# Kernel tuning notes

Hardware: AMD Instinct MI355X
Metric: run time of the kernel (lower is better)

Reference implementation:

```python
import jax, jax.numpy as jnp
import numpy as np

N, K, D = 131072, 1024, 128
COMMITMENT_COST = 0.25


def setup_inputs() -> dict:
    key = jax.random.key(0)
    k1, k2 = jax.random.split(key)
    c_input = jax.random.normal(k1, (N, D), dtype=jnp.float32)
    # nn.Embedding weight initialized N(0, 0.1)
    embedding_weight = jax.random.normal(k2, (K, D), dtype=jnp.float32) * 0.1
    return {"c_input": c_input, "embedding_weight": embedding_weight}


def reference(c_input, embedding_weight):
    distances = (
        jnp.sum(c_input ** 2, axis=1, keepdims=True)
        + jnp.sum(embedding_weight ** 2, axis=1)
        - 2.0 * jnp.matmul(c_input, embedding_weight.T)
    )
    encoding_indices = jnp.argmin(distances, axis=1)  # [N]
    encodings = jax.nn.one_hot(encoding_indices, K, dtype=c_input.dtype)  # [N, K]
    # one-hot @ weight == direct gather
    quantized = embedding_weight[encoding_indices]  # [N, D]
    e_latent_loss = jnp.mean((jax.lax.stop_gradient(quantized) - c_input) ** 2)
    q_latent_loss = jnp.mean((quantized - jax.lax.stop_gradient(c_input)) ** 2)
    loss = q_latent_loss + COMMITMENT_COST * e_latent_loss
    # straight-through estimator
    quantized_st = c_input + jax.lax.stop_gradient(quantized - c_input)
    return (loss, quantized_st, encodings)
```

## Files before the change

kernel.cpp:

```cpp
#include <hip/hip_runtime.h>
#include <hip/hip_bf16.h>

#define NROWS 131072
#define KC 1024
#define DD 128
#define MARGIN 1e-3f

typedef __attribute__((ext_vector_type(8))) short short8;
typedef __attribute__((ext_vector_type(4))) float f32x4;

__device__ inline short f2bf_hi(float f) {
  unsigned u = __builtin_bit_cast(unsigned, f);
  u += 0x7fffu + ((u >> 16) & 1u);
  return (short)(u >> 16);
}
__device__ inline float bf2f(short s) {
  unsigned u = ((unsigned)(unsigned short)s) << 16;
  return __builtin_bit_cast(float, u);
}

__global__ void vq_prep(const float* __restrict__ E, short* __restrict__ EH,
                        short* __restrict__ EL, float* __restrict__ SE,
                        float* __restrict__ out) {
  int b = blockIdx.x, t = threadIdx.x;
  if (b < 64) {
    int idx = b * 256 + t;
    int s = (idx >> 6) & 3, l = idx & 63;
    int c = idx >> 8;
    int q = l >> 4, n = l & 15;
    const float* src = E + (16 * c + n) * DD + 32 * s + 8 * q;
    short8 h, lo;
#pragma unroll
    for (int j = 0; j < 8; ++j) {
      float x = src[j];
      short hb = f2bf_hi(x);
      h[j] = hb;
      lo[j] = f2bf_hi(x - bf2f(hb));
    }
    *(short8*)(EH + idx * 8) = h;
    *(short8*)(EL + idx * 8) = lo;
  } else {
    if (t == 0) out[0] = 0.f;
    for (int k = t; k < KC; k += 256) {
      double acc = 0.0;
      const float* er = E + k * DD;
      for (int i = 0; i < DD; ++i) { double v = (double)er[i]; acc += v * v; }
      SE[k] = (float)acc;
    }
  }
}

__global__ __launch_bounds__(256, 2) void vq_main(
    const float* __restrict__ X, const float* __restrict__ E,
    const short* __restrict__ EH, const short* __restrict__ EL,
    const float* __restrict__ SE, float* __restrict__ out) {
  __shared__ __align__(16) short lbh[16384];
  __shared__ __align__(16) short lbl[16384];
  __shared__ int lidx[128];
  __shared__ int lflag[128];
  __shared__ int lany;
  __shared__ float lx[128];
  __shared__ float lrv[256];
  __shared__ int lri[256];
  __shared__ float lsx;
  __shared__ float lloss[4];

  const int tid = threadIdx.x;
  const int w = tid >> 6, l = tid & 63, q = l >> 4, n = l & 15;
  const int row_base = blockIdx.x * 128;
  if (tid == 0) lany = 0;

  short8 ah[2][4], al[2][4];
#pragma unroll
  for (int mt = 0; mt < 2; ++mt) {
    const float* xp = X + (row_base + 32 * w + 16 * mt + n) * DD + 8 * q;
#pragma unroll
    for (int s = 0; s < 4; ++s) {
      f32x4 x0 = *(const f32x4*)(xp + 32 * s);
      f32x4 x1 = *(const f32x4*)(xp + 32 * s + 4);
#pragma unroll
      for (int j = 0; j < 4; ++j) {
        short hb = f2bf_hi(x0[j]);
        ah[mt][s][j] = hb;
        al[mt][s][j] = f2bf_hi(x0[j] - bf2f(hb));
        short hb2 = f2bf_hi(x1[j]);
        ah[mt][s][j + 4] = hb2;
        al[mt][s][j + 4] = f2bf_hi(x1[j] - bf2f(hb2));
      }
    }
  }

  float bestv[8], secv[8];
  int besti[8];
#pragma unroll
  for (int i = 0; i < 8; ++i) { bestv[i] = -3e38f; secv[i] = -3e38f; besti[i] = 0; }

  for (int cc = 0; cc < 8; ++cc) {
    {
      const short8* gh = (const short8*)(EH + cc * 16384);
      const short8* gl = (const short8*)(EL + cc * 16384);
      short8* dh = (short8*)lbh;
      short8* dl = (short8*)lbl;
#pragma unroll
      for (int i = 0; i < 4; ++i) {
        int u0 = i * 512 + tid;
        int u1 = u0 + 256;
        short8 a0 = gh[u0], a1 = gh[u1];
        short8 b0 = gl[u0], b1 = gl[u1];
        dh[u0] = a0; dh[u1] = a1;
        dl[u0] = b0; dl[u1] = b1;
      }
    }
    __syncthreads();

    f32x4 acc[2][8];
#pragma unroll
    for (int mt = 0; mt < 2; ++mt)
#pragma unroll
      for (int nt = 0; nt < 8; ++nt) acc[mt][nt] = (f32x4){0.f, 0.f, 0.f, 0.f};

#pragma unroll
    for (int nt = 0; nt < 8; ++nt) {
#pragma unroll
      for (int s = 0; s < 4; ++s) {
        short8 bh  = *(const short8*)(lbh + ((nt * 4 + s) * 64 + l) * 8);
        short8 blo = *(const short8*)(lbl + ((nt * 4 + s) * 64 + l) * 8);
        acc[0][nt] = __builtin_amdgcn_mfma_f32_16x16x32_bf16(ah[0][s], bh,  acc[0][nt], 0, 0, 0);
        acc[1][nt] = __builtin_amdgcn_mfma_f32_16x16x32_bf16(ah[1][s], bh,  acc[1][nt], 0, 0, 0);
        acc[0][nt] = __builtin_amdgcn_mfma_f32_16x16x32_bf16(al[0][s], bh,  acc[0][nt], 0, 0, 0);
        acc[1][nt] = __builtin_amdgcn_mfma_f32_16x16x32_bf16(al[1][s], bh,  acc[1][nt], 0, 0, 0);
        acc[0][nt] = __builtin_amdgcn_mfma_f32_16x16x32_bf16(ah[0][s], blo, acc[0][nt], 0, 0, 0);
        acc[1][nt] = __builtin_amdgcn_mfma_f32_16x16x32_bf16(ah[1][s], blo, acc[1][nt], 0, 0, 0);
      }
    }
    __syncthreads();

#pragma unroll
    for (int nt = 0; nt < 8; ++nt) {
      int k = cc * 128 + nt * 16 + n;
      float hse = 0.5f * SE[k];
#pragma unroll
      for (int mt = 0; mt < 2; ++mt)
#pragma unroll
        for (int r = 0; r < 4; ++r) {
          float sc = acc[mt][nt][r] - hse;
          int slot = mt * 4 + r;
          bool gt = sc > bestv[slot];
          secv[slot] = gt ? bestv[slot] : fmaxf(secv[slot], sc);
          if (gt) { bestv[slot] = sc; besti[slot] = k; }
        }
    }
  }

#pragma unroll
  for (int slot = 0; slot < 8; ++slot) {
    float v = bestv[slot], s2 = secv[slot];
    int bi = besti[slot];
#pragma unroll
    for (int m = 1; m <= 8; m <<= 1) {
      float v2 = __shfl_xor(v, m, 64);
      float sv2 = __shfl_xor(s2, m, 64);
      int i2 = __shfl_xor(bi, m, 64);
      float ns = fmaxf(fminf(v, v2), fmaxf(s2, sv2));
      if (v2 > v || (v2 == v && i2 < bi)) { v = v2; bi = i2; }
      s2 = ns;
    }
    if (n == 0) {
      int mt = slot >> 2, r = slot & 3;
      int rl = 32 * w + 16 * mt + 4 * q + r;
      int f = (v - s2) <= MARGIN;
      lidx[rl] = bi;
      lflag[rl] = f;
      if (f) lany = 1;
    }
  }
  __syncthreads();

  if (lany) {
    for (int rl = 0; rl < 128; ++rl) {
      if (lflag[rl] == 0) continue;
      if (tid < DD) lx[tid] = X[(row_base + rl) * DD + tid];
      __syncthreads();
      if (tid == 0) {
        double sx = 0.0;
        for (int i = 0; i < DD; ++i) { double v = (double)lx[i]; sx += v * v; }
        lsx = (float)sx;
      }
      __syncthreads();
      float dmin = 3e38f; int kmin = 0;
      for (int kk = tid; kk < KC; kk += 256) {
        double dot = 0.0;
        const float* er = E + kk * DD;
        for (int i = 0; i < DD; ++i) dot += (double)lx[i] * (double)er[i];
        float a = lsx + SE[kk];
        float b2 = (float)(2.0 * dot);
        float dnp = a - b2;
        if (dnp < dmin) { dmin = dnp; kmin = kk; }
      }
      lrv[tid] = dmin; lri[tid] = kmin;
      __syncthreads();
      if (tid == 0) {
        float dm = lrv[0]; int km = lri[0];
        for (int t2 = 1; t2 < 256; ++t2)
          if (lrv[t2] < dm || (lrv[t2] == dm && lri[t2] < km)) { dm = lrv[t2]; km = lri[t2]; }
        lidx[rl] = km;
      }
      __syncthreads();
    }
  }
  __syncthreads();

  float lp = 0.f;
  const int encb = 1 + NROWS * DD;
  for (int rl = w; rl < 128; rl += 4) {
    int row = row_base + rl;
    int idx = lidx[rl];
    float x0 = X[row * DD + l];
    float x1 = X[row * DD + 64 + l];
    float e0 = E[idx * DD + l];
    float e1 = E[idx * DD + 64 + l];
    float d0 = e0 - x0, d1 = e1 - x1;
    __builtin_nontemporal_store(x0 + d0, out + 1 + row * DD + l);
    __builtin_nontemporal_store(x1 + d1, out + 1 + row * DD + 64 + l);
    lp += d0 * d0 + d1 * d1;
    float* ob = out + encb + row * KC;
    if (l < 3) __builtin_nontemporal_store((l == idx) ? 1.f : 0.f, ob + l);
    for (int c = l; c < 255; c += 64) {
      int eb = 3 + 4 * c;
      f32x4 v;
      v[0] = (eb     == idx) ? 1.f : 0.f;
      v[1] = (eb + 1 == idx) ? 1.f : 0.f;
      v[2] = (eb + 2 == idx) ? 1.f : 0.f;
      v[3] = (eb + 3 == idx) ? 1.f : 0.f;
      __builtin_nontemporal_store(v, (f32x4*)(ob + eb));
    }
    if (l == 63) __builtin_nontemporal_store((1023 == idx) ? 1.f : 0.f, ob + 1023);
  }
#pragma unroll
  for (int m = 1; m < 64; m <<= 1) lp += __shfl_xor(lp, m, 64);
  if (l == 0) lloss[w] = lp;
  __syncthreads();
  if (tid == 0) {
    float t = (lloss[0] + lloss[1] + lloss[2] + lloss[3]) *
              (1.25f / ((float)NROWS * (float)DD));
    atomicAdd(out, t);
  }
}

extern "C" void kernel_launch(void* const* d_in, const int* in_sizes, int n_in,
                              void* d_out, int out_size, void* d_ws, size_t ws_size,
                              hipStream_t stream) {
  const float* X = (const float*)d_in[0];
  const float* E = (const float*)d_in[1];
  float* out = (float*)d_out;
  short* EH = (short*)d_ws;
  short* EL = EH + KC * DD;
  float* SE = (float*)(EL + KC * DD);
  vq_prep<<<65, 256, 0, stream>>>(E, EH, EL, SE, out);
  vq_main<<<NROWS / 128, 256, 0, stream>>>(X, E, EH, EL, SE, out);
}
```

Measured before the change: 854.4 us.

## Split argmin and output writing into separate kernels, halve codebook chunk

Splits the fused kernel in two. The first computes argmin indices with a smaller 64-code LDS chunk and fewer accumulators so three blocks fit per CU. The second streams the quantized output, the one-hot encodings and the loss across more blocks. The goal is to raise occupancy in the MFMA phase and give the write-bound phase its own launch, at the cost of an extra launch, an index round-trip through global memory, twice as many sync rounds, and X being read twice.

```diff
diff --git a/kernel.cpp b/kernel.cpp
--- a/kernel.cpp
+++ b/kernel.cpp
@@ -50,12 +50,12 @@
   }
 }
 
-__global__ __launch_bounds__(256, 2) void vq_main(
+__global__ __launch_bounds__(256, 3) void vq_argmin(
     const float* __restrict__ X, const float* __restrict__ E,
     const short* __restrict__ EH, const short* __restrict__ EL,
-    const float* __restrict__ SE, float* __restrict__ out) {
-  __shared__ __align__(16) short lbh[16384];
-  __shared__ __align__(16) short lbl[16384];
+    const float* __restrict__ SE, int* __restrict__ IDX) {
+  __shared__ __align__(16) short lbh[8192];
+  __shared__ __align__(16) short lbl[8192];
   __shared__ int lidx[128];
   __shared__ int lflag[128];
   __shared__ int lany;
@@ -63,7 +63,6 @@
   __shared__ float lrv[256];
   __shared__ int lri[256];
   __shared__ float lsx;
-  __shared__ float lloss[4];
 
   const int tid = threadIdx.x;
   const int w = tid >> 6, l = tid & 63, q = l >> 4, n = l & 15;
@@ -95,32 +94,29 @@
 #pragma unroll
   for (int i = 0; i < 8; ++i) { bestv[i] = -3e38f; secv[i] = -3e38f; besti[i] = 0; }
 
-  for (int cc = 0; cc < 8; ++cc) {
+  for (int cc = 0; cc < 16; ++cc) {
     {
-      const short8* gh = (const short8*)(EH + cc * 16384);
-      const short8* gl = (const short8*)(EL + cc * 16384);
+      const short8* gh = (const short8*)(EH + cc * 8192);
+      const short8* gl = (const short8*)(EL + cc * 8192);
       short8* dh = (short8*)lbh;
       short8* dl = (short8*)lbl;
 #pragma unroll
       for (int i = 0; i < 4; ++i) {
-        int u0 = i * 512 + tid;
-        int u1 = u0 + 256;
-        short8 a0 = gh[u0], a1 = gh[u1];
-        short8 b0 = gl[u0], b1 = gl[u1];
-        dh[u0] = a0; dh[u1] = a1;
-        dl[u0] = b0; dl[u1] = b1;
+        int u = i * 256 + tid;
+        dh[u] = gh[u];
+        dl[u] = gl[u];
       }
     }
     __syncthreads();
 
-    f32x4 acc[2][8];
+    f32x4 acc[2][4];
 #pragma unroll
     for (int mt = 0; mt < 2; ++mt)
 #pragma unroll
-      for (int nt = 0; nt < 8; ++nt) acc[mt][nt] = (f32x4){0.f, 0.f, 0.f, 0.f};
-
-#pragma unroll
-    for (int nt = 0; nt < 8; ++nt) {
+      for (int nt = 0; nt < 4; ++nt) acc[mt][nt] = (f32x4){0.f, 0.f, 0.f, 0.f};
+
+#pragma unroll
+    for (int nt = 0; nt < 4; ++nt) {
 #pragma unroll
       for (int s = 0; s < 4; ++s) {
         short8 bh  = *(const short8*)(lbh + ((nt * 4 + s) * 64 + l) * 8);
@@ -136,8 +132,8 @@
     __syncthreads();
 
 #pragma unroll
-    for (int nt = 0; nt < 8; ++nt) {
-      int k = cc * 128 + nt * 16 + n;
+    for (int nt = 0; nt < 4; ++nt) {
+      int k = cc * 64 + nt * 16 + n;
       float hse = 0.5f * SE[k];
 #pragma unroll
       for (int mt = 0; mt < 2; ++mt)
@@ -210,11 +206,22 @@
   }
   __syncthreads();
 
+  if (tid < 128) IDX[row_base + tid] = lidx[tid];
+}
+
+__global__ __launch_bounds__(256) void vq_out(
+    const float* __restrict__ X, const float* __restrict__ E,
+    const int* __restrict__ IDX, float* __restrict__ out) {
+  __shared__ float lloss[4];
+  const int tid = threadIdx.x;
+  const int w = tid >> 6, l = tid & 63;
+  const int row0 = blockIdx.x * 64 + w * 16;
+  const int encb = 1 + NROWS * DD;
+
   float lp = 0.f;
-  const int encb = 1 + NROWS * DD;
-  for (int rl = w; rl < 128; rl += 4) {
-    int row = row_base + rl;
-    int idx = lidx[rl];
+  for (int i = 0; i < 16; ++i) {
+    int row = row0 + i;
+    int idx = IDX[row];
     float x0 = X[row * DD + l];
     float x1 = X[row * DD + 64 + l];
     float e0 = E[idx * DD + l];
@@ -256,6 +263,8 @@
   short* EH = (short*)d_ws;
   short* EL = EH + KC * DD;
   float* SE = (float*)(EL + KC * DD);
+  int* IDX = (int*)(SE + KC);
   vq_prep<<<65, 256, 0, stream>>>(E, EH, EL, SE, out);
-  vq_main<<<NROWS / 128, 256, 0, stream>>>(X, E, EH, EL, SE, out);
-}
+  vq_argmin<<<NROWS / 128, 256, 0, stream>>>(X, E, EH, EL, SE, IDX);
+  vq_out<<<NROWS / 64, 256, 0, stream>>>(X, E, IDX, out);
+}
```

After: 925.9 us. +8.4%, slower.
